# Kernel optimization log

Measured on AMD Instinct MI355X. Metric: run time of the kernel, lower is better.

Reference implementation:

```python
import jax, jax.numpy as jnp
import numpy as np

C = 64      # in_planes == mid_planes == out_planes (see notes: required for shape consistency)
K = 16      # nsample == k (KNN neighbors)
N = 32768   # number of points
B = 1       # batch (forward only type-checks for B==1 or B==k)


def _bn(x, g, b):
    # inference-mode BatchNorm1d: running_mean=0, running_var=1, eps=1e-5; channel = last axis
    return x * (g / jnp.sqrt(1.0 + 1e-5)) + b


def setup_inputs():
    ks = jax.random.split(jax.random.key(0), 33)
    f = lambda i, s: jax.random.normal(ks[i], s, jnp.float32) * 0.05
    # neighbor indices: global indices into the flattened (B*N) point set; avoid self-loops
    # so degenerate zero-length edges (0/0 divisions) only occur with prob ~0
    rel = jax.random.randint(ks[3], (N, K), 1, N)
    idx = ((jnp.arange(N)[:, None] + rel) % N).reshape(B, N, K)
    return dict(
        x=jax.random.normal(ks[0], (B, C, N), jnp.float32),
        y=jax.random.normal(ks[1], (B, C, N), jnp.float32),
        y_xyz=jax.random.uniform(ks[2], (B, 3, N), dtype=jnp.float32),
        idx=idx,
        Wq=f(4, (C, C)), bq=f(5, (C,)),
        Wk=f(6, (C, C)), bk=f(7, (C,)),
        Wv=f(8, (C, C)), bv=f(9, (C,)),
        Wu=f(10, (C, 1)), bu=f(11, (1,)), gu=jnp.ones((1,), jnp.float32), bnu=f(12, (1,)),
        Wp1=f(13, (3, 3)), bp1=f(14, (3,)), gp=jnp.ones((3,), jnp.float32), bnp=f(15, (3,)),
        Wp2=f(16, (3, C)), bp2=f(17, (C,)),
        Wa1=f(18, (3, 3)), ba1=f(19, (3,)), ga=jnp.ones((3,), jnp.float32), bna=f(20, (3,)),
        Wa2=f(21, (3, C)), ba2=f(22, (C,)),
        gw1=jnp.ones((C,), jnp.float32), bw1b=f(23, (C,)), Ww1=f(24, (C, C)), bw1=f(25, (C,)),
        gw2=jnp.ones((C,), jnp.float32), bw2b=f(26, (C,)), Ww2=f(27, (C, C)), bw2=f(28, (C,)),
        a_p=f(29, (K, 1)), b_p=f(30, (K, C)), d_p=f(31, (K, C)),
    )


def reference(x, y, y_xyz, idx, Wq, bq, Wk, bk, Wv, bv, Wu, bu, gu, bnu,
              Wp1, bp1, gp, bnp, Wp2, bp2, Wa1, ba1, ga, bna, Wa2, ba2,
              gw1, bw1b, Ww1, bw1, gw2, bw2b, Ww2, bw2, a_p, b_p, d_p):
    b_, cin, n = x.shape
    p = jnp.transpose(y_xyz, (0, 2, 1)).reshape(b_ * n, 3)      # (N,3) coordinates
    y_r = jnp.transpose(y, (0, 2, 1))                            # (B,n,C)
    xt = jnp.transpose(x, (0, 2, 1)).reshape(b_ * n, cin)
    yt = y_r.reshape(b_ * n, cin)
    x_q = xt @ Wq + bq                                           # (N,C)
    y_k_all = yt @ Wk + bk                                       # (N,C)
    y_v_all = yt @ Wv + bv                                       # (N,C)
    # note: original uses x.reshape(-1, C) (NOT a transpose) -- kept faithfully
    x_uni = jax.nn.relu(_bn(x.reshape(-1, cin) @ Wu + bu, gu, bnu))  # (N,1)
    idxf = idx.reshape(b_ * n, -1)                               # (N,K) global neighbor idx
    pos = p[idxf] - p[:, None, :]                                # (N,K,3) relative coords
    y_kg = y_k_all[idxf]                                         # (N,K,C) gathered keys
    y_vg = y_v_all[idxf]                                         # (N,K,C) gathered values
    # distances computed on detached positions in the original (numpy round-trip)
    pos_sg = jax.lax.stop_gradient(pos)
    e_dis = jnp.linalg.norm(pos_sg, axis=2, keepdims=True)       # (N,K,1)
    e_dis_xy = jnp.linalg.norm(pos_sg[:, :, :2], axis=2, keepdims=True)
    cos_e = jnp.nan_to_num(e_dis_xy / e_dis)
    cos_a = jnp.nan_to_num(pos[:, :, 1:2] / e_dis_xy)
    all_feat = jnp.concatenate([e_dis, cos_a, cos_e], axis=-1)   # (N,K,3)
    all_feat = jax.nn.relu(_bn(all_feat @ Wa1 + ba1, ga, bna)) @ Wa2 + ba2  # (N,K,C)
    p_r = jax.nn.relu(_bn(pos @ Wp1 + bp1, gp, bnp)) @ Wp2 + bp2           # (N,K,C)
    p_r = p_r + d_p * all_feat
    # dual softmax attention
    diff = y_kg - x_q[:, None, :]                                # (N,K,C)
    w_d = jax.nn.softmax(jnp.einsum('nkc,n->ck', diff, x_uni[:, 0]), axis=1)  # (C,K)
    w_e = jax.nn.softmax(jnp.einsum('nc,ck->nk', y_r[0], w_d)[:, :, None], axis=1)  # (N,K,1)
    w = a_p * w_d.T[None] + b_p * w_e                            # (N,K,C)
    w = jax.nn.relu(_bn(w, gw1, bw1b)) @ Ww1 + bw1
    w = jax.nn.relu(_bn(w, gw2, bw2b)) @ Ww2 + bw2
    w = jax.nn.softmax(w, axis=1)                                # softmax over neighbors
    return ((y_vg + p_r) * w).sum(axis=1)                        # (N,C)
```

## Files before the change

kernel.cpp:

```cpp
#include <hip/hip_runtime.h>
#include <hip/hip_bf16.h>
#include <math.h>

#define NPTS 32768
#define C 64
#define K 16
#define NB2 512
#define NB2R 64
#define NTAB 512
#define XCH 8
#define BN_INV 0.99999500003749968f

__device__ __forceinline__ float safediv_n2n(float a, float b) {
    float q = a / b;
    if (isnan(q)) return 0.0f;
    if (isinf(q)) return copysignf(3.402823466e38f, q);
    return q;
}

__device__ __forceinline__ float bf16f(ushort u) {
    return __uint_as_float((unsigned)u << 16);
}

__global__ __launch_bounds__(256) void prep_kernel(
    const float* __restrict__ x, const float* __restrict__ y,
    const float* __restrict__ y_xyz,
    const float* __restrict__ Wk, const float* __restrict__ bk,
    const float* __restrict__ Wv, const float* __restrict__ bv,
    const float* __restrict__ Wu, const float* __restrict__ bu,
    const float* __restrict__ gu, const float* __restrict__ bnu,
    __hip_bfloat16* __restrict__ ykb, __hip_bfloat16* __restrict__ yvb,
    float* __restrict__ xu, float4* __restrict__ pk)
{
    const int dir  = blockIdx.y;
    const int lane = threadIdx.x & 63;
    const int wave = threadIdx.x >> 6;

    if (dir == 1) {
        const float wul = Wu[lane];
        const float bnscale = gu[0] * BN_INV;
        const float bu0 = bu[0], bnu0 = bnu[0];
        #pragma unroll 4
        for (int i = 0; i < 16; ++i) {
            const int m = blockIdx.x * 64 + wave * 16 + i;
            float v = x[m * 64 + lane] * wul;
            #pragma unroll
            for (int off = 32; off > 0; off >>= 1) v += __shfl_xor(v, off, 64);
            if (lane == 0) {
                float u = (v + bu0) * bnscale + bnu0;
                xu[m] = fmaxf(u, 0.0f);
            }
        }
        if (wave == 0) {
            const int p = blockIdx.x * 64 + lane;
            pk[p] = make_float4(y_xyz[p], y_xyz[NPTS + p], y_xyz[2 * NPTS + p], 0.0f);
        }
        return;
    }

    const float* __restrict__ W    = (dir == 0) ? Wk : Wv;
    const float* __restrict__ bias = (dir == 0) ? bk : bv;
    __hip_bfloat16* __restrict__ dst = (dir == 0) ? ykb : yvb;

    const int n0 = blockIdx.x * 64;
    __shared__ float hs[C][C];

    #pragma unroll
    for (int i = 0; i < 16; ++i) {
        const int c = i * 4 + wave;
        hs[c][lane] = y[(size_t)c * NPTS + n0 + lane];
    }
    __syncthreads();

    const int p0 = wave * 16;
    float acc[16];
    const float b = bias[lane];
    #pragma unroll
    for (int i = 0; i < 16; ++i) acc[i] = b;

    #pragma unroll
    for (int c = 0; c < C; ++c) {
        const float wcl = W[c * C + lane];
        float va[16];
        ((float4*)va)[0] = *(const float4*)&hs[c][p0];
        ((float4*)va)[1] = *(const float4*)&hs[c][p0 + 4];
        ((float4*)va)[2] = *(const float4*)&hs[c][p0 + 8];
        ((float4*)va)[3] = *(const float4*)&hs[c][p0 + 12];
        #pragma unroll
        for (int i = 0; i < 16; ++i) acc[i] = fmaf(va[i], wcl, acc[i]);
    }

    #pragma unroll
    for (int i = 0; i < 16; ++i)
        dst[(size_t)(n0 + p0 + i) * C + lane] = __float2bfloat16(acc[i]);
}

__global__ __launch_bounds__(256) void xvec_kernel(
    const float* __restrict__ x, const float* __restrict__ xu,
    float* __restrict__ xvecp)
{
    const int j  = blockIdx.x;
    const int ch = blockIdx.y;
    const int t  = threadIdx.x;
    const int nb = NPTS / XCH;
    const int n0 = ch * nb;
    float s = 0.0f;
    if (j < C) {
        const float* __restrict__ row = x + (size_t)j * NPTS + n0;
        const float* __restrict__ xr  = xu + n0;
        for (int n = t; n < nb; n += 256) s = fmaf(row[n], xr[n], s);
    } else {
        const float* __restrict__ xr = xu + n0;
        for (int n = t; n < nb; n += 256) s += xr[n];
    }
    __shared__ float red[256];
    red[t] = s;
    __syncthreads();
    #pragma unroll
    for (int off = 128; off > 0; off >>= 1) {
        if (t < off) red[t] += red[t + off];
        __syncthreads();
    }
    if (t == 0) xvecp[j * XCH + ch] = red[0];
}

__global__ __launch_bounds__(256) void sred_kernel(
    const __hip_bfloat16* __restrict__ ykb,
    const float* __restrict__ xu, const int* __restrict__ idx,
    float* __restrict__ partG)
{
    const int lane = threadIdx.x & 63;
    const int wv = __builtin_amdgcn_readfirstlane(threadIdx.x >> 6);
    const int gw = blockIdx.x * 4 + wv;
    const int nwv = NB2 * 4;
    const ushort* __restrict__ yku = (const ushort*)ykb;

    float g[K];
    #pragma unroll
    for (int k = 0; k < K; ++k) g[k] = 0.0f;

    for (int n = gw; n < NPTS; n += nwv) {
        const float xuv = xu[n];
        if (xuv != 0.0f) {
            const int4* ir = (const int4*)(idx + (size_t)n * K);
            const int4 i0 = ir[0], i1 = ir[1], i2 = ir[2], i3 = ir[3];
            int ids[K] = { i0.x, i0.y, i0.z, i0.w, i1.x, i1.y, i1.z, i1.w,
                           i2.x, i2.y, i2.z, i2.w, i3.x, i3.y, i3.z, i3.w };
            #pragma unroll
            for (int k = 0; k < K; ++k) {
                const float ykv = bf16f(yku[(size_t)ids[k] * C + lane]);
                g[k] = fmaf(ykv, xuv, g[k]);
            }
        }
    }

    __shared__ float red[4][K][C];
    #pragma unroll
    for (int k = 0; k < K; ++k) red[wv][k][lane] = g[k];
    __syncthreads();
    if (wv == 0) {
        #pragma unroll
        for (int k = 0; k < K; ++k) {
            float s = red[0][k][lane] + red[1][k][lane] + red[2][k][lane] + red[3][k][lane];
            partG[blockIdx.x * (K * C) + k * C + lane] = s;
        }
    }
}

__global__ __launch_bounds__(1024) void sred2_kernel(
    const float* __restrict__ partG, float* __restrict__ part2)
{
    const int j = blockIdx.x;
    const int t = threadIdx.x;
    float s = 0.0f;
    #pragma unroll
    for (int i = 0; i < NB2 / NB2R; ++i)
        s += partG[(size_t)(j + NB2R * i) * (K * C) + t];
    part2[(size_t)j * (K * C) + t] = s;
}

__global__ __launch_bounds__(1024) void wd_kernel(
    const float* __restrict__ part2, const float* __restrict__ xvecp,
    const float* __restrict__ Wq, const float* __restrict__ bq,
    const float* __restrict__ a_p,
    float* __restrict__ wd, float* __restrict__ awdT)
{
    __shared__ float S[K][C];
    __shared__ float xv[C + 1];
    __shared__ float T1s[C];
    const int t = threadIdx.x;
    const int c = t & 63;

    if (t < C + 1) {
        float s = 0.0f;
        #pragma unroll
        for (int ch = 0; ch < XCH; ++ch) s += xvecp[t * XCH + ch];
        xv[t] = s;
    }
    float s = 0.0f;
    #pragma unroll 8
    for (int b = 0; b < NB2R; ++b) s += part2[b * (K * C) + t];
    __syncthreads();

    if (t < C) {
        float t1 = bq[t] * xv[C];
        #pragma unroll 8
        for (int j = 0; j < C; ++j) t1 = fmaf(Wq[j * C + t], xv[j], t1);
        T1s[t] = t1;
    }
    __syncthreads();

    S[0][t] = s - T1s[c];
    __syncthreads();

    if (t < C) {
        float v[K];
        float m = -3.402823466e38f;
        #pragma unroll
        for (int k = 0; k < K; ++k) { v[k] = S[k][t]; m = fmaxf(m, v[k]); }
        float sum = 0.0f;
        #pragma unroll
        for (int k = 0; k < K; ++k) { v[k] = expf(v[k] - m); sum += v[k]; }
        const float r = 1.0f / sum;
        #pragma unroll
        for (int k = 0; k < K; ++k) {
            const float wv = v[k] * r;
            wd[t * K + k] = wv;
            awdT[k * C + t] = a_p[k] * wv;
        }
    }
}

__global__ __launch_bounds__(256) void we_kernel(
    const float* __restrict__ y, const float* __restrict__ wd,
    float* __restrict__ we)
{
    __shared__ float wds[C][K];
    const int lane = threadIdx.x & 63;
    const int wave = threadIdx.x >> 6;
    for (int i = threadIdx.x; i < C * K; i += 256) wds[0][i] = wd[i];
    __syncthreads();

    const int n = (blockIdx.x * 4 + wave) * 64 + lane;
    float L[K];
    #pragma unroll
    for (int k = 0; k < K; ++k) L[k] = 0.0f;
    for (int c = 0; c < C; ++c) {
        const float yv = y[c * NPTS + n];
        float wa[K];
        ((float4*)wa)[0] = ((const float4*)&wds[c][0])[0];
        ((float4*)wa)[1] = ((const float4*)&wds[c][0])[1];
        ((float4*)wa)[2] = ((const float4*)&wds[c][0])[2];
        ((float4*)wa)[3] = ((const float4*)&wds[c][0])[3];
        #pragma unroll
        for (int k = 0; k < K; ++k) L[k] = fmaf(yv, wa[k], L[k]);
    }
    float m = L[0];
    #pragma unroll
    for (int k = 1; k < K; ++k) m = fmaxf(m, L[k]);
    float sum = 0.0f;
    #pragma unroll
    for (int k = 0; k < K; ++k) { L[k] = expf(L[k] - m); sum += L[k]; }
    const float r = 1.0f / sum;
    float* dst = we + (size_t)n * K;
    ((float4*)dst)[0] = make_float4(L[0]*r, L[1]*r, L[2]*r, L[3]*r);
    ((float4*)dst)[1] = make_float4(L[4]*r, L[5]*r, L[6]*r, L[7]*r);
    ((float4*)dst)[2] = make_float4(L[8]*r, L[9]*r, L[10]*r, L[11]*r);
    ((float4*)dst)[3] = make_float4(L[12]*r, L[13]*r, L[14]*r, L[15]*r);
}

__global__ __launch_bounds__(64) void tab_kernel(
    const float* __restrict__ awdT, const float* __restrict__ b_p,
    const float* __restrict__ Ww1, const float* __restrict__ bw1,
    const float* __restrict__ Ww2, const float* __restrict__ bw2,
    const float* __restrict__ gw1, const float* __restrict__ bw1b,
    const float* __restrict__ gw2, const float* __restrict__ bw2b,
    float* __restrict__ tab)
{
    const int lane = threadIdx.x;
    const int k  = blockIdx.y;
    const int i0 = blockIdx.x * 16;

    const float aw = awdT[k * C + lane];
    const float bp = b_p[k * C + lane];
    const float gs1 = gw1[lane] * BN_INV, bb1 = bw1b[lane], bw1c = bw1[lane];
    const float gs2 = gw2[lane] * BN_INV, bb2 = bw2b[lane], bw2c = bw2[lane];

    float w1c[C], w2c[C];
    #pragma unroll
    for (int c = 0; c < C; ++c) { w1c[c] = Ww1[c * C + lane]; w2c[c] = Ww2[c * C + lane]; }

    __shared__ float hs[16][C];

    #pragma unroll
    for (int r = 0; r < 16; ++r) {
        const float t = (float)(i0 + r) * (1.0f / NTAB);
        const float wv = fmaf(bp, t, aw);
        hs[r][lane] = fmaxf(fmaf(wv, gs1, bb1), 0.0f);
    }
    __syncthreads();

    float o[16];
    #pragma unroll
    for (int r = 0; r < 16; ++r) o[r] = bw1c;
    #pragma unroll
    for (int c4 = 0; c4 < 16; ++c4) {
        #pragma unroll
        for (int r = 0; r < 16; ++r) {
            const float4 hv = *(const float4*)&hs[r][c4 * 4];
            o[r] = fmaf(hv.x, w1c[c4 * 4 + 0], o[r]);
            o[r] = fmaf(hv.y, w1c[c4 * 4 + 1], o[r]);
            o[r] = fmaf(hv.z, w1c[c4 * 4 + 2], o[r]);
            o[r] = fmaf(hv.w, w1c[c4 * 4 + 3], o[r]);
        }
    }
    __syncthreads();
    #pragma unroll
    for (int r = 0; r < 16; ++r)
        hs[r][lane] = fmaxf(fmaf(o[r], gs2, bb2), 0.0f);
    __syncthreads();
    #pragma unroll
    for (int r = 0; r < 16; ++r) o[r] = bw2c;
    #pragma unroll
    for (int c4 = 0; c4 < 16; ++c4) {
        #pragma unroll
        for (int r = 0; r < 16; ++r) {
            const float4 hv = *(const float4*)&hs[r][c4 * 4];
            o[r] = fmaf(hv.x, w2c[c4 * 4 + 0], o[r]);
            o[r] = fmaf(hv.y, w2c[c4 * 4 + 1], o[r]);
            o[r] = fmaf(hv.z, w2c[c4 * 4 + 2], o[r]);
            o[r] = fmaf(hv.w, w2c[c4 * 4 + 3], o[r]);
        }
    }
    #pragma unroll
    for (int r = 0; r < 16; ++r) {
        const int i = i0 + r;
        if (i <= NTAB) tab[(k * (NTAB + 1) + i) * C + lane] = o[r];
    }
}

__global__ __launch_bounds__(256, 5) void main4_kernel(
    const int* __restrict__ idx, const float4* __restrict__ pk,
    const __hip_bfloat16* __restrict__ yvb, const float* __restrict__ we,
    const float* __restrict__ tab, const float* __restrict__ d_p,
    const float* __restrict__ Wa1, const float* __restrict__ ba1,
    const float* __restrict__ ga, const float* __restrict__ bna,
    const float* __restrict__ Wa2, const float* __restrict__ ba2,
    const float* __restrict__ Wp1, const float* __restrict__ bp1,
    const float* __restrict__ gp, const float* __restrict__ bnp,
    const float* __restrict__ Wp2, const float* __restrict__ bp2,
    float* __restrict__ out)
{
    const int lane = threadIdx.x & 63;
    const int wv = __builtin_amdgcn_readfirstlane(threadIdx.x >> 6);
    const int n = blockIdx.x * 4 + wv;

    __shared__ float geo[4][K][8];
    __shared__ float prm[36];

    if (threadIdx.x < 36) {
        const int t = threadIdx.x;
        float v;
        if (t < 9)       v = Wa1[t];
        else if (t < 12) v = ba1[t - 9];
        else if (t < 21) v = Wp1[t - 12];
        else if (t < 24) v = bp1[t - 21];
        else if (t < 27) v = ga[t - 24];
        else if (t < 30) v = bna[t - 27];
        else if (t < 33) v = gp[t - 30];
        else             v = bnp[t - 33];
        prm[t] = v;
    }
    __syncthreads();

    const int4* ir = (const int4*)(idx + (size_t)n * K);
    const int4 i0 = ir[0], i1 = ir[1], i2 = ir[2], i3 = ir[3];
    const int ids[K] = { i0.x, i0.y, i0.z, i0.w, i1.x, i1.y, i1.z, i1.w,
                         i2.x, i2.y, i2.z, i2.w, i3.x, i3.y, i3.z, i3.w };
    const float4 self = pk[n];
    const float4 wv0 = ((const float4*)(we + (size_t)n * K))[0];
    const float4 wv1 = ((const float4*)(we + (size_t)n * K))[1];
    const float4 wv2 = ((const float4*)(we + (size_t)n * K))[2];
    const float4 wv3 = ((const float4*)(we + (size_t)n * K))[3];
    const float wearr[K] = { wv0.x, wv0.y, wv0.z, wv0.w, wv1.x, wv1.y, wv1.z, wv1.w,
                             wv2.x, wv2.y, wv2.z, wv2.w, wv3.x, wv3.y, wv3.z, wv3.w };

    const ushort* __restrict__ yvu_base = (const ushort*)yvb;
    ushort yvu[K];
    #pragma unroll
    for (int k = 0; k < K; ++k)
        yvu[k] = yvu_base[(size_t)ids[k] * C + lane];

    {
        const int idv = (idx + (size_t)n * K)[lane & 15];
        const float4 nb = pk[idv];
        const float px = nb.x - self.x;
        const float py = nb.y - self.y;
        const float pz = nb.z - self.z;
        const float ed  = sqrtf(px * px + py * py + pz * pz);
        const float exy = sqrtf(px * px + py * py);
        const float cose = safediv_n2n(exy, ed);
        const float cosa = safediv_n2n(py, exy);
        float gv[6];
        #pragma unroll
        for (int d = 0; d < 3; ++d) {
            const float a = ed * prm[d] + cosa * prm[3 + d] + cose * prm[6 + d] + prm[9 + d];
            gv[d] = fmaxf(a * (prm[24 + d] * BN_INV) + prm[27 + d], 0.0f);
            const float p = px * prm[12 + d] + py * prm[15 + d] + pz * prm[18 + d] + prm[21 + d];
            gv[3 + d] = fmaxf(p * (prm[30 + d] * BN_INV) + prm[33 + d], 0.0f);
        }
        if (lane < K) {
            float* g = &geo[wv][lane][0];
            g[1] = gv[0]; g[2] = gv[1]; g[3] = gv[2];
            g[4] = gv[3]; g[5] = gv[4]; g[6] = gv[5];
        }
    }

    float w2[K];
    #pragma unroll
    for (int h = 0; h < 2; ++h) {
        float tv0[8], tv1[8], fr[8];
        #pragma unroll
        for (int j = 0; j < 8; ++j) {
            const int k = h * 8 + j;
            const float u = wearr[k] * (float)NTAB;
            int ic = (int)u;
            ic = (ic < 0) ? 0 : (ic > NTAB - 1 ? NTAB - 1 : ic);
            fr[j] = u - (float)ic;
            const float* tp = tab + ((size_t)(k * (NTAB + 1) + ic) << 6) + lane;
            tv0[j] = tp[0];
            tv1[j] = tp[C];
        }
        #pragma unroll
        for (int j = 0; j < 8; ++j)
            w2[h * 8 + j] = fmaf(fr[j], tv1[j] - tv0[j], tv0[j]);
    }

    float m = w2[0];
    #pragma unroll
    for (int k = 1; k < K; ++k) m = fmaxf(m, w2[k]);
    float sum = 0.0f;
    #pragma unroll
    for (int k = 0; k < K; ++k) { w2[k] = __expf(w2[k] - m); sum += w2[k]; }
    const float r = 1.0f / sum;

    const float ba2c = ba2[lane], bp2c = bp2[lane];
    float wa2c[3], wp2c[3];
    #pragma unroll
    for (int d = 0; d < 3; ++d) { wa2c[d] = Wa2[d * C + lane]; wp2c[d] = Wp2[d * C + lane]; }

    float acc = 0.0f;
    #pragma unroll
    for (int k = 0; k < K; ++k) {
        const float4 g0 = *(const float4*)&geo[wv][k][0];
        const float4 g1 = *(const float4*)&geo[wv][k][4];
        const float afc = fmaf(g0.y, wa2c[0], fmaf(g0.z, wa2c[1], fmaf(g0.w, wa2c[2], ba2c)));
        float prc = fmaf(g1.x, wp2c[0], fmaf(g1.y, wp2c[1], fmaf(g1.z, wp2c[2], bp2c)));
        prc = fmaf(d_p[k * C + lane], afc, prc);
        acc = fmaf(bf16f(yvu[k]) + prc, w2[k] * r, acc);
    }
    out[(size_t)n * C + lane] = acc;
}

extern "C" void kernel_launch(void* const* d_in, const int* in_sizes, int n_in,
                              void* d_out, int out_size, void* d_ws, size_t ws_size,
                              hipStream_t stream)
{
    (void)in_sizes; (void)n_in; (void)out_size; (void)ws_size;
    const float* x     = (const float*)d_in[0];
    const float* y     = (const float*)d_in[1];
    const float* y_xyz = (const float*)d_in[2];
    const int*   idx   = (const int*)d_in[3];
    const float* Wq = (const float*)d_in[4];  const float* bq = (const float*)d_in[5];
    const float* Wk = (const float*)d_in[6];  const float* bk = (const float*)d_in[7];
    const float* Wv = (const float*)d_in[8];  const float* bv = (const float*)d_in[9];
    const float* Wu = (const float*)d_in[10]; const float* bu = (const float*)d_in[11];
    const float* gu = (const float*)d_in[12]; const float* bnu = (const float*)d_in[13];
    const float* Wp1 = (const float*)d_in[14]; const float* bp1 = (const float*)d_in[15];
    const float* gp  = (const float*)d_in[16]; const float* bnp = (const float*)d_in[17];
    const float* Wp2 = (const float*)d_in[18]; const float* bp2 = (const float*)d_in[19];
    const float* Wa1 = (const float*)d_in[20]; const float* ba1 = (const float*)d_in[21];
    const float* ga  = (const float*)d_in[22]; const float* bna = (const float*)d_in[23];
    const float* Wa2 = (const float*)d_in[24]; const float* ba2 = (const float*)d_in[25];
    const float* gw1 = (const float*)d_in[26]; const float* bw1b = (const float*)d_in[27];
    const float* Ww1 = (const float*)d_in[28]; const float* bw1 = (const float*)d_in[29];
    const float* gw2 = (const float*)d_in[30]; const float* bw2b = (const float*)d_in[31];
    const float* Ww2 = (const float*)d_in[32]; const float* bw2 = (const float*)d_in[33];
    const float* a_p = (const float*)d_in[34];
    const float* b_p = (const float*)d_in[35];
    const float* d_p = (const float*)d_in[36];
    float* out = (float*)d_out;

    float* ws = (float*)d_ws;
    float* we    = ws;
    float* tab   = ws + 2097152;
    __hip_bfloat16* ykb = (__hip_bfloat16*)(ws + 2622464);
    __hip_bfloat16* yvb = (__hip_bfloat16*)(ws + 3671040);
    float4* pk   = (float4*)(ws + 4719616);
    float* xu    = ws + 4850688;
    float* partG = ws + 4883456;
    float* part2 = ws + 5407744;
    float* wd    = ws + 5473280;
    float* awdT  = ws + 5474304;
    float* xvecp = ws + 5475328;

    prep_kernel<<<dim3(NPTS / 64, 3), 256, 0, stream>>>(
        x, y, y_xyz, Wk, bk, Wv, bv, Wu, bu, gu, bnu, ykb, yvb, xu, pk);
    xvec_kernel<<<dim3(C + 1, XCH), 256, 0, stream>>>(x, xu, xvecp);
    sred_kernel<<<NB2, 256, 0, stream>>>(ykb, xu, idx, partG);
    sred2_kernel<<<NB2R, 1024, 0, stream>>>(partG, part2);
    wd_kernel<<<1, 1024, 0, stream>>>(part2, xvecp, Wq, bq, a_p, wd, awdT);
    we_kernel<<<NPTS / 256, 256, 0, stream>>>(y, wd, we);
    tab_kernel<<<dim3(33, 16), 64, 0, stream>>>(awdT, b_p, Ww1, bw1, Ww2, bw2,
                                                gw1, bw1b, gw2, bw2b, tab);
    main4_kernel<<<NPTS / 4, 256, 0, stream>>>(idx, pk, yvb, we, tab, d_p,
        Wa1, ba1, ga, bna, Wa2, ba2, Wp1, bp1, gp, bnp, Wp2, bp2, out);
}
```

Measured before the change: 107.5 us.

## Merge independent reduction and table kernels into shared launches; widen sred grid

Folds xvec_kernel into the sred launch as extra trailing blocks, and we_kernel plus tab_kernel into one wetab launch that splits work by block index. This removes two kernel launches and lets independent work run side by side instead of back to back. NB2 grows from 512 to 2048 so the gather-heavy sred stage has more waves to hide latency. The cost is a larger partG buffer (the workspace is re-laid out to fit it) and more work in sred2, whose loop is now only partially unrolled.

Result: slower. 147.5 us (+37.3%).

```diff
diff --git a/kernel.cpp b/kernel.cpp
--- a/kernel.cpp
+++ b/kernel.cpp
@@ -5,7 +5,7 @@
 #define NPTS 32768
 #define C 64
 #define K 16
-#define NB2 512
+#define NB2 2048
 #define NB2R 64
 #define NTAB 512
 #define XCH 8
@@ -95,40 +95,42 @@
         dst[(size_t)(n0 + p0 + i) * C + lane] = __float2bfloat16(acc[i]);
 }
 
-__global__ __launch_bounds__(256) void xvec_kernel(
-    const float* __restrict__ x, const float* __restrict__ xu,
-    float* __restrict__ xvecp)
-{
-    const int j  = blockIdx.x;
-    const int ch = blockIdx.y;
-    const int t  = threadIdx.x;
-    const int nb = NPTS / XCH;
-    const int n0 = ch * nb;
-    float s = 0.0f;
-    if (j < C) {
-        const float* __restrict__ row = x + (size_t)j * NPTS + n0;
-        const float* __restrict__ xr  = xu + n0;
-        for (int n = t; n < nb; n += 256) s = fmaf(row[n], xr[n], s);
-    } else {
-        const float* __restrict__ xr = xu + n0;
-        for (int n = t; n < nb; n += 256) s += xr[n];
-    }
-    __shared__ float red[256];
-    red[t] = s;
-    __syncthreads();
-    #pragma unroll
-    for (int off = 128; off > 0; off >>= 1) {
-        if (t < off) red[t] += red[t + off];
+__global__ __launch_bounds__(256) void sredx_kernel(
+    const __hip_bfloat16* __restrict__ ykb,
+    const float* __restrict__ x,
+    const float* __restrict__ xu, const int* __restrict__ idx,
+    float* __restrict__ partG, float* __restrict__ xvecp)
+{
+    __shared__ float red[4][K][C];
+    __shared__ float xred[256];
+
+    if (blockIdx.x >= NB2) {
+        const int b  = blockIdx.x - NB2;
+        const int j  = b / XCH;
+        const int ch = b % XCH;
+        const int t  = threadIdx.x;
+        const int nb = NPTS / XCH;
+        const int n0 = ch * nb;
+        float s = 0.0f;
+        if (j < C) {
+            const float* __restrict__ row = x + (size_t)j * NPTS + n0;
+            const float* __restrict__ xr  = xu + n0;
+            for (int n = t; n < nb; n += 256) s = fmaf(row[n], xr[n], s);
+        } else {
+            const float* __restrict__ xr = xu + n0;
+            for (int n = t; n < nb; n += 256) s += xr[n];
+        }
+        xred[t] = s;
         __syncthreads();
-    }
-    if (t == 0) xvecp[j * XCH + ch] = red[0];
-}
-
-__global__ __launch_bounds__(256) void sred_kernel(
-    const __hip_bfloat16* __restrict__ ykb,
-    const float* __restrict__ xu, const int* __restrict__ idx,
-    float* __restrict__ partG)
-{
+        #pragma unroll
+        for (int off = 128; off > 0; off >>= 1) {
+            if (t < off) xred[t] += xred[t + off];
+            __syncthreads();
+        }
+        if (t == 0) xvecp[j * XCH + ch] = xred[0];
+        return;
+    }
+
     const int lane = threadIdx.x & 63;
     const int wv = __builtin_amdgcn_readfirstlane(threadIdx.x >> 6);
     const int gw = blockIdx.x * 4 + wv;
@@ -154,7 +156,6 @@
         }
     }
 
-    __shared__ float red[4][K][C];
     #pragma unroll
     for (int k = 0; k < K; ++k) red[wv][k][lane] = g[k];
     __syncthreads();
@@ -173,7 +174,7 @@
     const int j = blockIdx.x;
     const int t = threadIdx.x;
     float s = 0.0f;
-    #pragma unroll
+    #pragma unroll 8
     for (int i = 0; i < NB2 / NB2R; ++i)
         s += partG[(size_t)(j + NB2R * i) * (K * C) + t];
     part2[(size_t)j * (K * C) + t] = s;
@@ -231,55 +232,57 @@
     }
 }
 
-__global__ __launch_bounds__(256) void we_kernel(
+__global__ __launch_bounds__(256) void wetab_kernel(
     const float* __restrict__ y, const float* __restrict__ wd,
-    float* __restrict__ we)
-{
-    __shared__ float wds[C][K];
-    const int lane = threadIdx.x & 63;
-    const int wave = threadIdx.x >> 6;
-    for (int i = threadIdx.x; i < C * K; i += 256) wds[0][i] = wd[i];
-    __syncthreads();
-
-    const int n = (blockIdx.x * 4 + wave) * 64 + lane;
-    float L[K];
-    #pragma unroll
-    for (int k = 0; k < K; ++k) L[k] = 0.0f;
-    for (int c = 0; c < C; ++c) {
-        const float yv = y[c * NPTS + n];
-        float wa[K];
-        ((float4*)wa)[0] = ((const float4*)&wds[c][0])[0];
-        ((float4*)wa)[1] = ((const float4*)&wds[c][0])[1];
-        ((float4*)wa)[2] = ((const float4*)&wds[c][0])[2];
-        ((float4*)wa)[3] = ((const float4*)&wds[c][0])[3];
-        #pragma unroll
-        for (int k = 0; k < K; ++k) L[k] = fmaf(yv, wa[k], L[k]);
-    }
-    float m = L[0];
-    #pragma unroll
-    for (int k = 1; k < K; ++k) m = fmaxf(m, L[k]);
-    float sum = 0.0f;
-    #pragma unroll
-    for (int k = 0; k < K; ++k) { L[k] = expf(L[k] - m); sum += L[k]; }
-    const float r = 1.0f / sum;
-    float* dst = we + (size_t)n * K;
-    ((float4*)dst)[0] = make_float4(L[0]*r, L[1]*r, L[2]*r, L[3]*r);
-    ((float4*)dst)[1] = make_float4(L[4]*r, L[5]*r, L[6]*r, L[7]*r);
-    ((float4*)dst)[2] = make_float4(L[8]*r, L[9]*r, L[10]*r, L[11]*r);
-    ((float4*)dst)[3] = make_float4(L[12]*r, L[13]*r, L[14]*r, L[15]*r);
-}
-
-__global__ __launch_bounds__(64) void tab_kernel(
     const float* __restrict__ awdT, const float* __restrict__ b_p,
     const float* __restrict__ Ww1, const float* __restrict__ bw1,
     const float* __restrict__ Ww2, const float* __restrict__ bw2,
     const float* __restrict__ gw1, const float* __restrict__ bw1b,
     const float* __restrict__ gw2, const float* __restrict__ bw2b,
-    float* __restrict__ tab)
-{
-    const int lane = threadIdx.x;
-    const int k  = blockIdx.y;
-    const int i0 = blockIdx.x * 16;
+    float* __restrict__ we, float* __restrict__ tab)
+{
+    __shared__ float smem[4 * 16 * C];
+    const int lane = threadIdx.x & 63;
+    const int wave = threadIdx.x >> 6;
+
+    if (blockIdx.x < 128) {
+        float* wds = smem;
+        for (int i = threadIdx.x; i < C * K; i += 256) wds[i] = wd[i];
+        __syncthreads();
+
+        const int n = (blockIdx.x * 4 + wave) * 64 + lane;
+        float L[K];
+        #pragma unroll
+        for (int k = 0; k < K; ++k) L[k] = 0.0f;
+        for (int c = 0; c < C; ++c) {
+            const float yv = y[c * NPTS + n];
+            float wa[K];
+            ((float4*)wa)[0] = ((const float4*)&wds[c * K])[0];
+            ((float4*)wa)[1] = ((const float4*)&wds[c * K])[1];
+            ((float4*)wa)[2] = ((const float4*)&wds[c * K])[2];
+            ((float4*)wa)[3] = ((const float4*)&wds[c * K])[3];
+            #pragma unroll
+            for (int k = 0; k < K; ++k) L[k] = fmaf(yv, wa[k], L[k]);
+        }
+        float m = L[0];
+        #pragma unroll
+        for (int k = 1; k < K; ++k) m = fmaxf(m, L[k]);
+        float sum = 0.0f;
+        #pragma unroll
+        for (int k = 0; k < K; ++k) { L[k] = expf(L[k] - m); sum += L[k]; }
+        const float r = 1.0f / sum;
+        float* dst = we + (size_t)n * K;
+        ((float4*)dst)[0] = make_float4(L[0]*r, L[1]*r, L[2]*r, L[3]*r);
+        ((float4*)dst)[1] = make_float4(L[4]*r, L[5]*r, L[6]*r, L[7]*r);
+        ((float4*)dst)[2] = make_float4(L[8]*r, L[9]*r, L[10]*r, L[11]*r);
+        ((float4*)dst)[3] = make_float4(L[12]*r, L[13]*r, L[14]*r, L[15]*r);
+        return;
+    }
+
+    const int gwv = (blockIdx.x - 128) * 4 + wave;
+    const int k  = gwv / 33;
+    const int i0 = (gwv % 33) * 16;
+    float* hs = smem + wave * 16 * C;
 
     const float aw = awdT[k * C + lane];
     const float bp = b_p[k * C + lane];
@@ -290,13 +293,11 @@
     #pragma unroll
     for (int c = 0; c < C; ++c) { w1c[c] = Ww1[c * C + lane]; w2c[c] = Ww2[c * C + lane]; }
 
-    __shared__ float hs[16][C];
-
     #pragma unroll
     for (int r = 0; r < 16; ++r) {
         const float t = (float)(i0 + r) * (1.0f / NTAB);
         const float wv = fmaf(bp, t, aw);
-        hs[r][lane] = fmaxf(fmaf(wv, gs1, bb1), 0.0f);
+        hs[r * C + lane] = fmaxf(fmaf(wv, gs1, bb1), 0.0f);
     }
     __syncthreads();
 
@@ -307,7 +308,7 @@
     for (int c4 = 0; c4 < 16; ++c4) {
         #pragma unroll
         for (int r = 0; r < 16; ++r) {
-            const float4 hv = *(const float4*)&hs[r][c4 * 4];
+            const float4 hv = *(const float4*)&hs[r * C + c4 * 4];
             o[r] = fmaf(hv.x, w1c[c4 * 4 + 0], o[r]);
             o[r] = fmaf(hv.y, w1c[c4 * 4 + 1], o[r]);
             o[r] = fmaf(hv.z, w1c[c4 * 4 + 2], o[r]);
@@ -317,7 +318,7 @@
     __syncthreads();
     #pragma unroll
     for (int r = 0; r < 16; ++r)
-        hs[r][lane] = fmaxf(fmaf(o[r], gs2, bb2), 0.0f);
+        hs[r * C + lane] = fmaxf(fmaf(o[r], gs2, bb2), 0.0f);
     __syncthreads();
     #pragma unroll
     for (int r = 0; r < 16; ++r) o[r] = bw2c;
@@ -325,7 +326,7 @@
     for (int c4 = 0; c4 < 16; ++c4) {
         #pragma unroll
         for (int r = 0; r < 16; ++r) {
-            const float4 hv = *(const float4*)&hs[r][c4 * 4];
+            const float4 hv = *(const float4*)&hs[r * C + c4 * 4];
             o[r] = fmaf(hv.x, w2c[c4 * 4 + 0], o[r]);
             o[r] = fmaf(hv.y, w2c[c4 * 4 + 1], o[r]);
             o[r] = fmaf(hv.z, w2c[c4 * 4 + 2], o[r]);
@@ -493,12 +494,12 @@
 
     float* ws = (float*)d_ws;
     float* we    = ws;
-    float* tab   = ws + 2097152;
-    __hip_bfloat16* ykb = (__hip_bfloat16*)(ws + 2622464);
-    __hip_bfloat16* yvb = (__hip_bfloat16*)(ws + 3671040);
-    float4* pk   = (float4*)(ws + 4719616);
-    float* xu    = ws + 4850688;
-    float* partG = ws + 4883456;
+    float* tab   = ws + 524288;
+    __hip_bfloat16* ykb = (__hip_bfloat16*)(ws + 1049600);
+    __hip_bfloat16* yvb = (__hip_bfloat16*)(ws + 2098176);
+    float4* pk   = (float4*)(ws + 3146752);
+    float* xu    = ws + 3277824;
+    float* partG = ws + 3310592;
     float* part2 = ws + 5407744;
     float* wd    = ws + 5473280;
     float* awdT  = ws + 5474304;
@@ -506,13 +507,12 @@
 
     prep_kernel<<<dim3(NPTS / 64, 3), 256, 0, stream>>>(
         x, y, y_xyz, Wk, bk, Wv, bv, Wu, bu, gu, bnu, ykb, yvb, xu, pk);
-    xvec_kernel<<<dim3(C + 1, XCH), 256, 0, stream>>>(x, xu, xvecp);
-    sred_kernel<<<NB2, 256, 0, stream>>>(ykb, xu, idx, partG);
+    sredx_kernel<<<NB2 + (C + 1) * XCH, 256, 0, stream>>>(
+        ykb, x, xu, idx, partG, xvecp);
     sred2_kernel<<<NB2R, 1024, 0, stream>>>(partG, part2);
     wd_kernel<<<1, 1024, 0, stream>>>(part2, xvecp, Wq, bq, a_p, wd, awdT);
-    we_kernel<<<NPTS / 256, 256, 0, stream>>>(y, wd, we);
-    tab_kernel<<<dim3(33, 16), 64, 0, stream>>>(awdT, b_p, Ww1, bw1, Ww2, bw2,
-                                                gw1, bw1b, gw2, bw2b, tab);
+    wetab_kernel<<<128 + 132, 256, 0, stream>>>(
+        y, wd, awdT, b_p, Ww1, bw1, Ww2, bw2, gw1, bw1b, gw2, bw2b, we, tab);
     main4_kernel<<<NPTS / 4, 256, 0, stream>>>(idx, pk, yvb, we, tab, d_p,
         Wa1, ba1, ga, bna, Wa2, ba2, Wp1, bp1, gp, bnp, Wp2, bp2, out);
 }
```
